# Performance work log

Hardware: AMD Instinct MI355X
Metric: run time of the kernel (lower is better)

## Reference

```python
import jax, jax.numpy as jnp
import numpy as np

SEQ, B, D_MODEL, NHEAD = 256, 128, 512, 8
HID = 3 * D_MODEL  # GRUCell hidden size


def setup_inputs() -> dict:
    key = jax.random.key(0)
    ks = jax.random.split(key, 7)
    s_g = 1.0 / np.sqrt(HID)        # torch GRUCell init: U(-1/sqrt(hidden), 1/sqrt(hidden))
    s_o = 1.0 / np.sqrt(D_MODEL)    # torch Linear init
    u = lambda k, shp, s: jax.random.uniform(k, shp, jnp.float32, -s, s)
    return {
        "x": jax.random.normal(ks[0], (SEQ, B, D_MODEL), jnp.float32),
        "Wih": u(ks[1], (3 * HID, 2 * D_MODEL), s_g),
        "Whh": u(ks[2], (3 * HID, HID), s_g),
        "bih": u(ks[3], (3 * HID,), s_g),
        "bhh": u(ks[4], (3 * HID,), s_g),
        "Wo": u(ks[5], (D_MODEL, D_MODEL), s_o),
        "bo": u(ks[6], (D_MODEL,), s_o),
    }


def _unitnorm(v):
    return v / jnp.linalg.norm(v, axis=-1, keepdims=True)


def _unitelu(v):
    return jax.nn.elu(_unitnorm(v))


def _gru_cell(xr, h, Wih, Whh, bih, bhh):
    gi = xr @ Wih.T + bih
    gh = h @ Whh.T + bhh
    ir, iz, inn = jnp.split(gi, 3, axis=-1)
    hr, hz, hn = jnp.split(gh, 3, axis=-1)
    rg = jax.nn.sigmoid(ir + hr)
    zg = jax.nn.sigmoid(iz + hz)
    n = jnp.tanh(inn + rg * hn)
    return (1.0 - zg) * n + zg * h


def reference(x, Wih, Whh, bih, bhh, Wo, bo):
    Bsz, d = x.shape[1], x.shape[2]
    nh, dim = NHEAD, d // NHEAD
    dt = x.dtype

    def step(carry, x_i):
        h, r, A, _, _ = carry
        xr = jnp.concatenate([x_i, r], axis=-1)           # [B, 2d]
        h = _gru_cell(xr, h, Wih, Whh, bih, bhh)          # [B, 3d]
        k = _unitelu(h[:, d:2 * d].reshape(Bsz, nh, dim))
        v = h[:, 2 * d:3 * d].reshape(Bsz, nh, dim)
        A = A + jnp.einsum('bnq,bnv->bnvq', k, v)         # fast-weight accumulation
        q = _unitnorm(h[:, :d].reshape(Bsz, nh, dim))
        r = jnp.einsum('bnq,bnvq->bnv', q, A).reshape(Bsz, -1)
        return (h, r, A, k, q), None

    init = (
        jnp.zeros((Bsz, HID), dt),            # h (torch GRUCell defaults hidden to zeros)
        jnp.zeros((Bsz, d), dt),              # r
        jnp.zeros((Bsz, nh, dim, dim), dt),   # A
        jnp.zeros((Bsz, nh, dim), dt),        # k (last)
        jnp.zeros((Bsz, nh, dim), dt),        # q (last)
    )
    (h, r, A, k, q), _ = jax.lax.scan(step, init, x)
    out = r @ Wo.T + bo
    return out, k, q
```

## Files before the change

### kernel.cpp

```cpp
#include <hip/hip_runtime.h>
#include <hip/hip_bf16.h>

#define SEQ  256
#define BSZ  128
#define DM   512
#define HID  1536
#define KTOT 2560
#define VC   6144
#define NBLK 720

typedef __attribute__((ext_vector_type(4))) float f32x4;
typedef __attribute__((ext_vector_type(8))) short short8;
typedef __attribute__((ext_vector_type(4))) unsigned short us4;
typedef __attribute__((ext_vector_type(8))) unsigned short us8;
typedef __attribute__((ext_vector_type(4))) unsigned int u32x4;

#define OFF_WBH 0ull
#define OFF_P   47185920ull
#define OFF_R32 62914560ull
#define OFF_RBH 80740352ull
#define OFF_HBH 81002496ull
#define OFF_BAR 81788928ull

static __device__ __forceinline__ unsigned short bf(float x) {
  __hip_bfloat16 h = __float2bfloat16(x);
  return *reinterpret_cast<unsigned short*>(&h);
}

static __device__ __forceinline__ void stf_llc(float* p, float v) {
  asm volatile("global_store_dword %0, %1, off sc0 sc1" :: "v"(p), "v"(v) : "memory");
}
static __device__ __forceinline__ void st16_llc(unsigned short* p, unsigned short v) {
  unsigned vv = v;
  asm volatile("global_store_short %0, %1, off sc0 sc1" :: "v"(p), "v"(vv) : "memory");
}
static __device__ __forceinline__ float ldf_llc(const float* p) {
  return __hip_atomic_load(p, __ATOMIC_RELAXED, __HIP_MEMORY_SCOPE_SYSTEM);
}
static __device__ __forceinline__ void ld1x16_llc(const unsigned short* p, u32x4& r0) {
  asm volatile(
      "global_load_dwordx4 %0, %1, off sc0 sc1\n\t"
      "s_waitcnt vmcnt(0)"
      : "=&v"(r0) : "v"(p) : "memory");
}
static __device__ __forceinline__ unsigned sysld(unsigned* p) {
  return __hip_atomic_load(p, __ATOMIC_RELAXED, __HIP_MEMORY_SCOPE_SYSTEM);
}

static __device__ __forceinline__ void gsync(unsigned* bar) {
  asm volatile("s_waitcnt vmcnt(0)" ::: "memory");
  __syncthreads();
  if (threadIdx.x == 0) {
    unsigned* root = bar;
    unsigned* ep   = bar + 32;
    unsigned* gcnt = bar + 64 + (blockIdx.x >> 4) * 16;
    unsigned e = sysld(ep);
    if (atomicAdd(gcnt, 1u) == 15u) {
      atomicSub(gcnt, 16u);
      if (atomicAdd(root, 1u) == 44u) {
        atomicSub(root, 45u);
        atomicAdd(ep, 1u);
      }
    }
    while (sysld(ep) == e) __builtin_amdgcn_s_sleep(8);
  }
  __syncthreads();
}

__global__ __launch_bounds__(256) void pk_wb(const float* __restrict__ Wih,
                                             const float* __restrict__ Whh,
                                             unsigned short* __restrict__ Wh,
                                             unsigned* __restrict__ bar) {
  if (blockIdx.x == 0)
    for (int i = threadIdx.x; i < 1024; i += 256) bar[i] = 0u;
  int idx = blockIdx.x * 256 + threadIdx.x;
  int row = idx / 640;
  int k = (idx - row * 640) * 4;
  const float* src = (k < 1024) ? (Wih + (size_t)row * 1024 + k)
                                : (Whh + (size_t)row * HID + (k - 1024));
  f32x4 v = *(const f32x4*)src;
  us4 oh;
#pragma unroll
  for (int i = 0; i < 4; ++i) oh[i] = bf(v[i]);
  *(us4*)(Wh + (size_t)row * KTOT + k) = oh;
}

__global__ __launch_bounds__(256) void pk_zero(f32x4* __restrict__ dst) {
  f32x4 z = {0.f, 0.f, 0.f, 0.f};
  dst[(size_t)blockIdx.x * 256 + threadIdx.x] = z;
}

__global__ __launch_bounds__(256, 3) void fused(
    const float* __restrict__ x, const float* __restrict__ bih,
    const float* __restrict__ bhh, char* __restrict__ ws,
    float* __restrict__ dout)
{
  const unsigned short* Wh = (const unsigned short*)(ws + OFF_WBH);
  float*          P   = (float*)(ws + OFF_P);
  float*          r32 = (float*)(ws + OFF_R32);
  unsigned short* Rbh = (unsigned short*)(ws + OFF_RBH);
  unsigned short* Hbh = (unsigned short*)(ws + OFF_HBH);
  unsigned* bar = (unsigned*)(ws + OFF_BAR);

  const int blk = blockIdx.x;
  const int tid = threadIdx.x;

  unsigned xcd;
  asm volatile("s_getreg_b32 %0, hwreg(HW_REG_XCC_ID)" : "=s"(xcd));
  xcd &= 7;
  __shared__ unsigned rankS;
  if (tid == 0) rankS = atomicAdd(&bar[832 + xcd * 16], 1u);
  __syncthreads();
  const unsigned rank = rankS;

  const int wave = tid >> 6, lane = tid & 63;
  const int jh  = wave * 16;
  const int l15 = lane & 15, kg = lane >> 4;
  const int sr_ = tid >> 2;
  const int sc_ = (tid & 3) * 8;

  __shared__ __align__(16) unsigned short AH[64 * 40];
  __shared__ __align__(16) float Alds[2][64 * 65];
  __shared__ float kS[2][64];
  __shared__ float qS[2][64];

  for (int i = tid; i < 2 * 64 * 65; i += 256) ((float*)Alds)[i] = 0.f;
  float hprev[3] = {0.f, 0.f, 0.f};
  gsync(bar);
  const unsigned cnt_g = sysld(&bar[832 + xcd * 16]);

  for (int t = 0; t < SEQ; ++t) {
    for (unsigned v = rank; v < 90u; v += cnt_g) {
      int jg, ks, half;
      if (v < 60u)      { jg = 6 * xcd + v / 10;                unsigned r = v % 10; ks = r >> 1; half = r & 1; }
      else if (v < 72u) { unsigned w = v - 60; jg = 48 + 3 * xcd + w / 4; unsigned r = w % 4; ks = r >> 1;       half = r & 1; }
      else              { unsigned w = v - 72; jg = 72 + 3 * xcd + w / 6; unsigned r = w % 6; ks = 2 + (r >> 1); half = r & 1; }
      int colb, wrowb;
      if (jg < 48)      { colb = jg * 64;               wrowb = colb; }
      else if (jg < 72) { colb = 3072 + (jg - 48) * 64; wrowb = colb; }
      else              { colb = 4608 + (jg - 72) * 64; wrowb = colb - 1536; }
      const int kc0 = ks * 512;
      const int b0g = half * 64;
      const int wrow0 = wrowb + jh;

      f32x4 acc[4];
#pragma unroll
      for (int i = 0; i < 4; ++i) acc[i] = (f32x4){0.f, 0.f, 0.f, 0.f};

      for (int it = 0; it < 16; ++it) {
        int kabs = kc0 + it * 32;
        us8 h0;
        u32x4 a0;
        if (ks == 0) {
          const float* p = x + ((size_t)(t * BSZ + b0g + sr_)) * DM + kabs + sc_;
          f32x4 f0 = ((const f32x4*)p)[0];
          f32x4 f1 = ((const f32x4*)p)[1];
#pragma unroll
          for (int i = 0; i < 4; ++i) {
            h0[i]     = bf(f0[i]);
            h0[4 + i] = bf(f1[i]);
          }
        } else if (ks == 1) {
          size_t off = (size_t)(b0g + sr_) * DM + (kabs - 512) + sc_;
          ld1x16_llc(Rbh + off, a0);
        } else {
          size_t off = (size_t)(b0g + sr_) * HID + (kabs - 1024) + sc_;
          ld1x16_llc(Hbh + off, a0);
        }
        __syncthreads();
        if (ks == 0) *(us8*)&AH[sr_ * 40 + sc_]   = h0;
        else         *(u32x4*)&AH[sr_ * 40 + sc_] = a0;
        __syncthreads();

        size_t woff = (size_t)(wrow0 + l15) * KTOT + kabs + kg * 8;
        short8 wh_ = *(const short8*)(Wh + woff);
#pragma unroll
        for (int bt = 0; bt < 4; ++bt) {
          short8 ah = *(const short8*)&AH[(bt * 16 + l15) * 40 + kg * 8];
          acc[bt] = __builtin_amdgcn_mfma_f32_16x16x32_bf16(ah, wh_, acc[bt], 0, 0, 0);
        }
      }
#pragma unroll
      for (int bt = 0; bt < 4; ++bt)
#pragma unroll
        for (int i = 0; i < 4; ++i)
          stf_llc(&P[((size_t)ks * BSZ + b0g + bt * 16 + kg * 4 + i) * VC + colb + jh + l15],
                  acc[bt][i]);
    }
    gsync(bar);

    if (blk < 512 && wave < 2) {
      const int pair = blk * 2 + wave;
      const int b = pair >> 3, n = pair & 7;
      const int l = lane;
      const float* Pb = P + (size_t)b * VC;
      float hv[3];
#pragma unroll
      for (int s = 0; s < 3; ++s) {
        int c = s * 512 + n * 64 + l;
        float sr2 = 0.f, sz = 0.f;
#pragma unroll
        for (int ksi = 0; ksi < 5; ++ksi) {
          const float* q = Pb + (size_t)ksi * BSZ * VC;
          sr2 += ldf_llc(q + c);
          sz  += ldf_llc(q + 1536 + c);
        }
        float gin = ldf_llc(Pb + 3072 + c) + ldf_llc(Pb + (size_t)BSZ * VC + 3072 + c);
        float ghn = 0.f;
#pragma unroll
        for (int ksi = 2; ksi < 5; ++ksi)
          ghn += ldf_llc(Pb + (size_t)ksi * BSZ * VC + 4608 + c);
        float rg = 1.f / (1.f + __expf(-(sr2 + bih[c] + bhh[c])));
        float zg = 1.f / (1.f + __expf(-(sz + bih[1536 + c] + bhh[1536 + c])));
        float nn = tanhf(gin + bih[3072 + c] + rg * (ghn + bhh[3072 + c]));
        float hnew = (1.f - zg) * nn + zg * hprev[s];
        hprev[s] = hnew;
        size_t hix = (size_t)b * HID + c;
        st16_llc(&Hbh[hix], bf(hnew));
        hv[s] = hnew;
      }
      float ssq = hv[0] * hv[0], ssk = hv[1] * hv[1];
#pragma unroll
      for (int off = 32; off > 0; off >>= 1) {
        ssq += __shfl_xor(ssq, off);
        ssk += __shfl_xor(ssk, off);
      }
      float qn = hv[0] * rsqrtf(ssq);
      float kn = hv[1] * rsqrtf(ssk);
      float ke = kn > 0.f ? kn : expm1f(kn);
      kS[wave][l] = ke;
      qS[wave][l] = qn;

      float vvl = hv[2];
      float* Arow = &Alds[wave][l * 65];
      float racc = 0.f;
#pragma unroll
      for (int q4 = 0; q4 < 16; ++q4) {
        float a0 = Arow[q4 * 4 + 0], a1 = Arow[q4 * 4 + 1];
        float a2 = Arow[q4 * 4 + 2], a3 = Arow[q4 * 4 + 3];
        float k0 = kS[wave][q4 * 4 + 0], k1 = kS[wave][q4 * 4 + 1];
        float k2 = kS[wave][q4 * 4 + 2], k3 = kS[wave][q4 * 4 + 3];
        float q0 = qS[wave][q4 * 4 + 0], q1 = qS[wave][q4 * 4 + 1];
        float q2 = qS[wave][q4 * 4 + 2], q3 = qS[wave][q4 * 4 + 3];
        a0 += k0 * vvl; a1 += k1 * vvl; a2 += k2 * vvl; a3 += k3 * vvl;
        racc += q0 * a0 + q1 * a1 + q2 * a2 + q3 * a3;
        Arow[q4 * 4 + 0] = a0; Arow[q4 * 4 + 1] = a1;
        Arow[q4 * 4 + 2] = a2; Arow[q4 * 4 + 3] = a3;
      }
      size_t ri = (size_t)b * DM + n * 64 + l;
      st16_llc(&Rbh[ri], bf(racc));

      if (t == SEQ - 1) {
        r32[ri] = racc;
        dout[65536  + pair * 64 + l] = ke;
        dout[131072 + pair * 64 + l] = qn;
      }
    }
    gsync(bar);
  }
}

__global__ __launch_bounds__(512) void out_gemm(const float* __restrict__ r32,
                                                const float* __restrict__ Wo,
                                                const float* __restrict__ bo,
                                                float* __restrict__ dout) {
  int b0 = blockIdx.x * 2;
  int o  = threadIdx.x;
  __shared__ float rL0[512];
  __shared__ float rL1[512];
  rL0[o] = r32[(size_t)b0 * DM + o];
  rL1[o] = r32[(size_t)(b0 + 1) * DM + o];
  __syncthreads();
  float a0 = bo[o], a1 = a0;
  const float* wrow = Wo + (size_t)o * DM;
  for (int c = 0; c < DM; ++c) {
    float w = wrow[c];
    a0 += rL0[c] * w;
    a1 += rL1[c] * w;
  }
  dout[(size_t)b0 * DM + o]       = a0;
  dout[(size_t)(b0 + 1) * DM + o] = a1;
}

extern "C" void kernel_launch(void* const* d_in, const int* in_sizes, int n_in,
                              void* d_out, int out_size, void* d_ws, size_t ws_size,
                              hipStream_t stream) {
  int ix = 0, iwih = 1, iwhh = 2, ibih = 3, ibhh = 4, iwo = 5, ibo = 6;
  {
    int b1 = -1, b2 = -1;
    for (int i = 0; i < n_in; ++i) {
      int s = in_sizes[i];
      if      (s == SEQ * BSZ * DM) ix = i;
      else if (s == 4608 * 1024)    iwih = i;
      else if (s == 4608 * 1536)    iwhh = i;
      else if (s == DM * DM)        iwo = i;
      else if (s == DM)             ibo = i;
      else if (s == 4608)           { if (b1 < 0) b1 = i; else b2 = i; }
    }
    if (b1 >= 0) ibih = b1;
    if (b2 >= 0) ibhh = b2;
  }
  const float* x   = (const float*)d_in[ix];
  const float* Wih = (const float*)d_in[iwih];
  const float* Whh = (const float*)d_in[iwhh];
  const float* bih = (const float*)d_in[ibih];
  const float* bhh = (const float*)d_in[ibhh];
  const float* Wo  = (const float*)d_in[iwo];
  const float* bo  = (const float*)d_in[ibo];

  char* ws = (char*)d_ws;
  unsigned short* Wh  = (unsigned short*)(ws + OFF_WBH);
  float*          r32 = (float*)(ws + OFF_R32);
  unsigned*       bar = (unsigned*)(ws + OFF_BAR);
  float* dout = (float*)d_out;

  pk_wb  <<<11520, 256, 0, stream>>>(Wih, Whh, Wh, bar);
  pk_zero<<<256,   256, 0, stream>>>((f32x4*)(ws + OFF_RBH));
  fused  <<<NBLK,  256, 0, stream>>>(x, bih, bhh, ws, dout);
  out_gemm<<<64, 512, 0, stream>>>(r32, Wo, bo, dout);
}
```

Measured before the change: 7.611 ms.

## Software-pipeline GEMM tile loads with double-buffered LDS and prefetch depth two

Replaces the per-iteration load, wait, and two-barrier GEMM inner loop with a two-deep prefetch pipeline. Activation and weight loads for iteration it+2 are issued as inline asm while iteration it computes, and partial s_waitcnt counts gate consumption. The LDS staging buffer is doubled so writes for the next step do not race with reads of the current one. This hides global/LLC load latency inside the recurrent step, but relies on hand-managed vmcnt accounting and raises register pressure.

Measured after the change: 7.102 ms. 1.07x faster.

```diff
diff --git a/kernel.cpp b/kernel.cpp
--- a/kernel.cpp
+++ b/kernel.cpp
@@ -37,15 +37,24 @@
 static __device__ __forceinline__ float ldf_llc(const float* p) {
   return __hip_atomic_load(p, __ATOMIC_RELAXED, __HIP_MEMORY_SCOPE_SYSTEM);
 }
-static __device__ __forceinline__ void ld1x16_llc(const unsigned short* p, u32x4& r0) {
-  asm volatile(
-      "global_load_dwordx4 %0, %1, off sc0 sc1\n\t"
-      "s_waitcnt vmcnt(0)"
-      : "=&v"(r0) : "v"(p) : "memory");
-}
 static __device__ __forceinline__ unsigned sysld(unsigned* p) {
   return __hip_atomic_load(p, __ATOMIC_RELAXED, __HIP_MEMORY_SCOPE_SYSTEM);
 }
+
+#define ISSUE_B(j, a_, w_)                                              \
+  asm volatile("global_load_dwordx4 %0, %2, off sc0 sc1\n\t"           \
+               "global_load_dwordx4 %1, %3, off"                        \
+               : "=&v"(a_), "=&v"(w_)                                   \
+               : "v"(actbase + (j) * 32), "v"(wbase + (j) * 32)         \
+               : "memory");
+#define ISSUE_X(j, f0_, f1_, w_)                                        \
+  asm volatile("global_load_dwordx4 %0, %3, off sc0 sc1\n\t"           \
+               "global_load_dwordx4 %1, %4, off sc0 sc1\n\t"           \
+               "global_load_dwordx4 %2, %5, off"                        \
+               : "=&v"(f0_), "=&v"(f1_), "=&v"(w_)                      \
+               : "v"(xbase + (j) * 32), "v"(xbase + (j) * 32 + 4),      \
+                 "v"(wbase + (j) * 32)                                  \
+               : "memory");
 
 static __device__ __forceinline__ void gsync(unsigned* bar) {
   asm volatile("s_waitcnt vmcnt(0)" ::: "memory");
@@ -119,7 +128,7 @@
   const int sr_ = tid >> 2;
   const int sc_ = (tid & 3) * 8;
 
-  __shared__ __align__(16) unsigned short AH[64 * 40];
+  __shared__ __align__(16) unsigned short AH[2][64 * 40];
   __shared__ __align__(16) float Alds[2][64 * 65];
   __shared__ float kS[2][64];
   __shared__ float qS[2][64];
@@ -143,43 +152,81 @@
       const int b0g = half * 64;
       const int wrow0 = wrowb + jh;
 
+      const unsigned short* wbase = Wh + (size_t)(wrow0 + l15) * KTOT + kc0 + kg * 8;
+
       f32x4 acc[4];
 #pragma unroll
       for (int i = 0; i < 4; ++i) acc[i] = (f32x4){0.f, 0.f, 0.f, 0.f};
 
-      for (int it = 0; it < 16; ++it) {
-        int kabs = kc0 + it * 32;
-        us8 h0;
-        u32x4 a0;
-        if (ks == 0) {
-          const float* p = x + ((size_t)(t * BSZ + b0g + sr_)) * DM + kabs + sc_;
-          f32x4 f0 = ((const f32x4*)p)[0];
-          f32x4 f1 = ((const f32x4*)p)[1];
+      asm volatile("s_waitcnt vmcnt(0)" ::: "memory");
+
+      if (ks == 0) {
+        const float* xbase = x + ((size_t)(t * BSZ + b0g + sr_)) * DM + kc0 + sc_;
+        u32x4 fA0, fA1, wA, fB0, fB1, wB;
+        ISSUE_X(0, fA0, fA1, wA);
+        ISSUE_X(1, fB0, fB1, wB);
+#pragma unroll
+        for (int it = 0; it < 16; ++it) {
+          if (it < 15) asm volatile("s_waitcnt vmcnt(3)" ::: "memory");
+          else         asm volatile("s_waitcnt vmcnt(0)" ::: "memory");
+          __builtin_amdgcn_sched_barrier(0);
+          const int sl = it & 1;
+          f32x4 f0 = sl ? *(f32x4*)&fB0 : *(f32x4*)&fA0;
+          f32x4 f1 = sl ? *(f32x4*)&fB1 : *(f32x4*)&fA1;
+          us8 h0;
 #pragma unroll
           for (int i = 0; i < 4; ++i) {
             h0[i]     = bf(f0[i]);
             h0[4 + i] = bf(f1[i]);
           }
-        } else if (ks == 1) {
-          size_t off = (size_t)(b0g + sr_) * DM + (kabs - 512) + sc_;
-          ld1x16_llc(Rbh + off, a0);
-        } else {
-          size_t off = (size_t)(b0g + sr_) * HID + (kabs - 1024) + sc_;
-          ld1x16_llc(Hbh + off, a0);
+          *(us8*)&AH[sl][sr_ * 40 + sc_] = h0;
+          asm volatile("s_waitcnt lgkmcnt(0)" ::: "memory");
+          __builtin_amdgcn_s_barrier();
+          __builtin_amdgcn_sched_barrier(0);
+          short8 wh_ = sl ? *(short8*)&wB : *(short8*)&wA;
+#pragma unroll
+          for (int bt = 0; bt < 4; ++bt) {
+            short8 ah = *(const short8*)&AH[sl][(bt * 16 + l15) * 40 + kg * 8];
+            acc[bt] = __builtin_amdgcn_mfma_f32_16x16x32_bf16(ah, wh_, acc[bt], 0, 0, 0);
+          }
+          if (it < 14) {
+            if (sl) { ISSUE_X(it + 2, fB0, fB1, wB); }
+            else    { ISSUE_X(it + 2, fA0, fA1, wA); }
+          }
+          __builtin_amdgcn_s_barrier();
         }
-        __syncthreads();
-        if (ks == 0) *(us8*)&AH[sr_ * 40 + sc_]   = h0;
-        else         *(u32x4*)&AH[sr_ * 40 + sc_] = a0;
-        __syncthreads();
-
-        size_t woff = (size_t)(wrow0 + l15) * KTOT + kabs + kg * 8;
-        short8 wh_ = *(const short8*)(Wh + woff);
-#pragma unroll
-        for (int bt = 0; bt < 4; ++bt) {
-          short8 ah = *(const short8*)&AH[(bt * 16 + l15) * 40 + kg * 8];
-          acc[bt] = __builtin_amdgcn_mfma_f32_16x16x32_bf16(ah, wh_, acc[bt], 0, 0, 0);
+      } else {
+        const unsigned short* actbase =
+            (ks == 1) ? (Rbh + (size_t)(b0g + sr_) * DM + (kc0 - 512) + sc_)
+                      : (Hbh + (size_t)(b0g + sr_) * HID + (kc0 - 1024) + sc_);
+        u32x4 aA, wA, aB, wB;
+        ISSUE_B(0, aA, wA);
+        ISSUE_B(1, aB, wB);
+#pragma unroll
+        for (int it = 0; it < 16; ++it) {
+          if (it < 15) asm volatile("s_waitcnt vmcnt(2)" ::: "memory");
+          else         asm volatile("s_waitcnt vmcnt(0)" ::: "memory");
+          __builtin_amdgcn_sched_barrier(0);
+          const int sl = it & 1;
+          u32x4 av = sl ? aB : aA;
+          *(u32x4*)&AH[sl][sr_ * 40 + sc_] = av;
+          asm volatile("s_waitcnt lgkmcnt(0)" ::: "memory");
+          __builtin_amdgcn_s_barrier();
+          __builtin_amdgcn_sched_barrier(0);
+          short8 wh_ = sl ? *(short8*)&wB : *(short8*)&wA;
+#pragma unroll
+          for (int bt = 0; bt < 4; ++bt) {
+            short8 ah = *(const short8*)&AH[sl][(bt * 16 + l15) * 40 + kg * 8];
+            acc[bt] = __builtin_amdgcn_mfma_f32_16x16x32_bf16(ah, wh_, acc[bt], 0, 0, 0);
+          }
+          if (it < 14) {
+            if (sl) { ISSUE_B(it + 2, aB, wB); }
+            else    { ISSUE_B(it + 2, aA, wA); }
+          }
+          __builtin_amdgcn_s_barrier();
         }
       }
+
 #pragma unroll
       for (int bt = 0; bt < 4; ++bt)
 #pragma unroll
```

## Double-buffer GEMM tile loads per wave and drop block-wide syncs

Applied to the files above, without the earlier changes.

Restructures the per-step GEMM tile so each wave owns 16 batch rows and all 64 output columns, staging its activations in a private LDS slice instead of a block-shared tile. This removes the two __syncthreads per k-iteration. Loads of activations and weights are issued two iterations ahead with inline asm and a register double buffer, using explicit vmcnt waits so memory latency overlaps the MFMAs. In exchange each wave now loads four weight fragments per iteration instead of one, and the kernel relies on hand-managed wait counts.

After: 12.03 ms. 1.58x slower.

```diff
diff --git a/kernel.cpp b/kernel.cpp
--- a/kernel.cpp
+++ b/kernel.cpp
@@ -37,15 +37,38 @@
 static __device__ __forceinline__ float ldf_llc(const float* p) {
   return __hip_atomic_load(p, __ATOMIC_RELAXED, __HIP_MEMORY_SCOPE_SYSTEM);
 }
-static __device__ __forceinline__ void ld1x16_llc(const unsigned short* p, u32x4& r0) {
-  asm volatile(
-      "global_load_dwordx4 %0, %1, off sc0 sc1\n\t"
-      "s_waitcnt vmcnt(0)"
-      : "=&v"(r0) : "v"(p) : "memory");
-}
 static __device__ __forceinline__ unsigned sysld(unsigned* p) {
   return __hip_atomic_load(p, __ATOMIC_RELAXED, __HIP_MEMORY_SCOPE_SYSTEM);
 }
+
+#define ISS_B(a_, w0_, w1_, w2_, w3_, j)                                   \
+  asm volatile("global_load_dwordx4 %0, %5, off sc0 sc1\n\t"              \
+               "global_load_dwordx4 %1, %6, off\n\t"                       \
+               "global_load_dwordx4 %2, %7, off\n\t"                       \
+               "global_load_dwordx4 %3, %8, off\n\t"                       \
+               "global_load_dwordx4 %4, %9, off"                           \
+               : "=&v"(a_), "=&v"(w0_), "=&v"(w1_), "=&v"(w2_), "=&v"(w3_) \
+               : "v"(actbase + (j) * 32), "v"(wb0 + (j) * 32),             \
+                 "v"(wb1 + (j) * 32), "v"(wb2 + (j) * 32),                 \
+                 "v"(wb3 + (j) * 32)                                       \
+               : "memory");
+#define ISS_X(f0_, f1_, w0_, w1_, w2_, w3_, j)                             \
+  asm volatile("global_load_dwordx4 %0, %6, off sc0 sc1\n\t"              \
+               "global_load_dwordx4 %1, %7, off sc0 sc1\n\t"              \
+               "global_load_dwordx4 %2, %8, off\n\t"                       \
+               "global_load_dwordx4 %3, %9, off\n\t"                       \
+               "global_load_dwordx4 %4, %10, off\n\t"                      \
+               "global_load_dwordx4 %5, %11, off"                          \
+               : "=&v"(f0_), "=&v"(f1_), "=&v"(w0_), "=&v"(w1_),           \
+                 "=&v"(w2_), "=&v"(w3_)                                    \
+               : "v"(xbase + (j) * 32), "v"(xbase + (j) * 32 + 4),         \
+                 "v"(wb0 + (j) * 32), "v"(wb1 + (j) * 32),                 \
+                 "v"(wb2 + (j) * 32), "v"(wb3 + (j) * 32)                  \
+               : "memory");
+
+#define WAITV(N)                                                           \
+  asm volatile("s_waitcnt vmcnt(" #N ")" ::: "memory");                    \
+  __builtin_amdgcn_sched_barrier(0);
 
 static __device__ __forceinline__ void gsync(unsigned* bar) {
   asm volatile("s_waitcnt vmcnt(0)" ::: "memory");
@@ -114,12 +137,12 @@
   const unsigned rank = rankS;
 
   const int wave = tid >> 6, lane = tid & 63;
-  const int jh  = wave * 16;
   const int l15 = lane & 15, kg = lane >> 4;
-  const int sr_ = tid >> 2;
-  const int sc_ = (tid & 3) * 8;
-
-  __shared__ __align__(16) unsigned short AH[64 * 40];
+  const int bw16 = wave * 16;
+  const int srow = lane >> 2;
+  const int scol = (lane & 3) * 8;
+
+  __shared__ __align__(16) unsigned short SB[4][2][16 * 36];
   __shared__ __align__(16) float Alds[2][64 * 65];
   __shared__ float kS[2][64];
   __shared__ float qS[2][64];
@@ -141,51 +164,90 @@
       else              { colb = 4608 + (jg - 72) * 64; wrowb = colb - 1536; }
       const int kc0 = ks * 512;
       const int b0g = half * 64;
-      const int wrow0 = wrowb + jh;
-
-      f32x4 acc[4];
-#pragma unroll
-      for (int i = 0; i < 4; ++i) acc[i] = (f32x4){0.f, 0.f, 0.f, 0.f};
-
-      for (int it = 0; it < 16; ++it) {
-        int kabs = kc0 + it * 32;
-        us8 h0;
-        u32x4 a0;
-        if (ks == 0) {
-          const float* p = x + ((size_t)(t * BSZ + b0g + sr_)) * DM + kabs + sc_;
-          f32x4 f0 = ((const f32x4*)p)[0];
-          f32x4 f1 = ((const f32x4*)p)[1];
+
+      const unsigned short* wb0 = Wh + (size_t)(wrowb + l15) * KTOT + kc0 + kg * 8;
+      const unsigned short* wb1 = wb0 + (size_t)16 * KTOT;
+      const unsigned short* wb2 = wb0 + (size_t)32 * KTOT;
+      const unsigned short* wb3 = wb0 + (size_t)48 * KTOT;
+      unsigned short* sb0 = &SB[wave][0][0];
+      unsigned short* sb1 = &SB[wave][1][0];
+
+      f32x4 acc0 = {0.f,0.f,0.f,0.f}, acc1 = {0.f,0.f,0.f,0.f};
+      f32x4 acc2 = {0.f,0.f,0.f,0.f}, acc3 = {0.f,0.f,0.f,0.f};
+
+      asm volatile("s_waitcnt vmcnt(0)" ::: "memory");
+
+      if (ks == 0) {
+        const float* xbase = x + ((size_t)(t * BSZ + b0g + bw16 + srow)) * DM + kc0 + scol;
+        u32x4 fA0, fA1, wA0, wA1, wA2, wA3, fB0, fB1, wB0, wB1, wB2, wB3;
+        ISS_X(fA0, fA1, wA0, wA1, wA2, wA3, 0);
+        ISS_X(fB0, fB1, wB0, wB1, wB2, wB3, 1);
+#pragma unroll
+        for (int it = 0; it < 16; ++it) {
+          if (it < 15) { WAITV(6) } else { WAITV(0) }
+          const int sl = it & 1;
+          f32x4 f0 = sl ? *(f32x4*)&fB0 : *(f32x4*)&fA0;
+          f32x4 f1 = sl ? *(f32x4*)&fB1 : *(f32x4*)&fA1;
+          us8 h0;
 #pragma unroll
           for (int i = 0; i < 4; ++i) {
             h0[i]     = bf(f0[i]);
             h0[4 + i] = bf(f1[i]);
           }
-        } else if (ks == 1) {
-          size_t off = (size_t)(b0g + sr_) * DM + (kabs - 512) + sc_;
-          ld1x16_llc(Rbh + off, a0);
-        } else {
-          size_t off = (size_t)(b0g + sr_) * HID + (kabs - 1024) + sc_;
-          ld1x16_llc(Hbh + off, a0);
+          unsigned short* sb = sl ? sb1 : sb0;
+          *(us8*)&sb[srow * 36 + scol] = h0;
+          short8 ah = *(const short8*)&sb[l15 * 36 + kg * 8];
+          short8 w0 = sl ? *(short8*)&wB0 : *(short8*)&wA0;
+          short8 w1 = sl ? *(short8*)&wB1 : *(short8*)&wA1;
+          short8 w2 = sl ? *(short8*)&wB2 : *(short8*)&wA2;
+          short8 w3 = sl ? *(short8*)&wB3 : *(short8*)&wA3;
+          acc0 = __builtin_amdgcn_mfma_f32_16x16x32_bf16(ah, w0, acc0, 0, 0, 0);
+          acc1 = __builtin_amdgcn_mfma_f32_16x16x32_bf16(ah, w1, acc1, 0, 0, 0);
+          acc2 = __builtin_amdgcn_mfma_f32_16x16x32_bf16(ah, w2, acc2, 0, 0, 0);
+          acc3 = __builtin_amdgcn_mfma_f32_16x16x32_bf16(ah, w3, acc3, 0, 0, 0);
+          if (it < 14) {
+            if (sl) { ISS_X(fB0, fB1, wB0, wB1, wB2, wB3, it + 2) }
+            else    { ISS_X(fA0, fA1, wA0, wA1, wA2, wA3, it + 2) }
+          }
         }
-        __syncthreads();
-        if (ks == 0) *(us8*)&AH[sr_ * 40 + sc_]   = h0;
-        else         *(u32x4*)&AH[sr_ * 40 + sc_] = a0;
-        __syncthreads();
-
-        size_t woff = (size_t)(wrow0 + l15) * KTOT + kabs + kg * 8;
-        short8 wh_ = *(const short8*)(Wh + woff);
-#pragma unroll
-        for (int bt = 0; bt < 4; ++bt) {
-          short8 ah = *(const short8*)&AH[(bt * 16 + l15) * 40 + kg * 8];
-          acc[bt] = __builtin_amdgcn_mfma_f32_16x16x32_bf16(ah, wh_, acc[bt], 0, 0, 0);
+      } else {
+        const unsigned short* actbase =
+            (ks == 1) ? (Rbh + (size_t)(b0g + bw16 + srow) * DM + (kc0 - 512) + scol)
+                      : (Hbh + (size_t)(b0g + bw16 + srow) * HID + (kc0 - 1024) + scol);
+        u32x4 aA, wA0, wA1, wA2, wA3, aB, wB0, wB1, wB2, wB3;
+        ISS_B(aA, wA0, wA1, wA2, wA3, 0);
+        ISS_B(aB, wB0, wB1, wB2, wB3, 1);
+#pragma unroll
+        for (int it = 0; it < 16; ++it) {
+          if (it < 15) { WAITV(5) } else { WAITV(0) }
+          const int sl = it & 1;
+          u32x4 av = sl ? aB : aA;
+          unsigned short* sb = sl ? sb1 : sb0;
+          *(u32x4*)&sb[srow * 36 + scol] = av;
+          short8 ah = *(const short8*)&sb[l15 * 36 + kg * 8];
+          short8 w0 = sl ? *(short8*)&wB0 : *(short8*)&wA0;
+          short8 w1 = sl ? *(short8*)&wB1 : *(short8*)&wA1;
+          short8 w2 = sl ? *(short8*)&wB2 : *(short8*)&wA2;
+          short8 w3 = sl ? *(short8*)&wB3 : *(short8*)&wA3;
+          acc0 = __builtin_amdgcn_mfma_f32_16x16x32_bf16(ah, w0, acc0, 0, 0, 0);
+          acc1 = __builtin_amdgcn_mfma_f32_16x16x32_bf16(ah, w1, acc1, 0, 0, 0);
+          acc2 = __builtin_amdgcn_mfma_f32_16x16x32_bf16(ah, w2, acc2, 0, 0, 0);
+          acc3 = __builtin_amdgcn_mfma_f32_16x16x32_bf16(ah, w3, acc3, 0, 0, 0);
+          if (it < 14) {
+            if (sl) { ISS_B(aB, wB0, wB1, wB2, wB3, it + 2) }
+            else    { ISS_B(aA, wA0, wA1, wA2, wA3, it + 2) }
+          }
         }
       }
-#pragma unroll
-      for (int bt = 0; bt < 4; ++bt)
-#pragma unroll
-        for (int i = 0; i < 4; ++i)
-          stf_llc(&P[((size_t)ks * BSZ + b0g + bt * 16 + kg * 4 + i) * VC + colb + jh + l15],
-                  acc[bt][i]);
+
+      float* Pw = P + ((size_t)ks * BSZ + b0g + bw16 + kg * 4) * VC + colb + l15;
+#pragma unroll
+      for (int i = 0; i < 4; ++i) {
+        stf_llc(Pw + (size_t)i * VC,      acc0[i]);
+        stf_llc(Pw + (size_t)i * VC + 16, acc1[i]);
+        stf_llc(Pw + (size_t)i * VC + 32, acc2[i]);
+        stf_llc(Pw + (size_t)i * VC + 48, acc3[i]);
+      }
     }
     gsync(bar);
 
```
